# Performance work log

Measured on AMD Instinct MI355X. Metric: run time of the kernel, lower is better.

Reference implementation:

```python
import jax, jax.numpy as jnp
import numpy as np
import math

NUM_HEADS = 16
HEAD_SIZE = 64
SEQ_LEN = 2048
D_MODEL = NUM_HEADS * HEAD_SIZE
BATCH = 2


def _xavier(key, shape):
    fan_in, fan_out = shape[0], shape[1]
    limit = math.sqrt(6.0 / (fan_in + fan_out))
    return jax.random.uniform(key, shape, jnp.float32, -limit, limit)


def setup_inputs() -> dict:
    key = jax.random.key(0)
    ks = jax.random.split(key, 5)
    x = jax.random.normal(ks[0], (BATCH, SEQ_LEN, D_MODEL), jnp.float32)
    W_Q = _xavier(ks[1], (D_MODEL, D_MODEL))
    W_K = _xavier(ks[2], (D_MODEL, D_MODEL))
    W_V = _xavier(ks[3], (D_MODEL, D_MODEL))
    W_O = _xavier(ks[4], (D_MODEL, D_MODEL))
    zeros = jnp.zeros((D_MODEL,), jnp.float32)
    return {
        "x": x,
        "W_Q": W_Q, "W_K": W_K, "W_V": W_V, "W_O": W_O,
        "b_Q": zeros, "b_K": zeros, "b_V": zeros, "b_O": zeros,
    }


def _split_heads(t):
    # [B, S, H*d] -> [B, H, S, d]
    B, S, _ = t.shape
    return t.reshape(B, S, NUM_HEADS, HEAD_SIZE).transpose(0, 2, 1, 3)


def reference(x, W_Q, W_K, W_V, W_O, b_Q, b_K, b_V, b_O):
    q = _split_heads(x @ W_Q + b_Q)  # [B,H,S,d]
    k = _split_heads(x @ W_K + b_K)
    v = _split_heads(x @ W_V + b_V)

    # scores: [B,H,S,S]
    scores = jnp.einsum("bhqd,bhkd->bhqk", q, k)
    # Faithful to original: multiply by lower-triangular 0/1 mask, scale,
    # then add -10000 on strictly-upper positions (NOT -inf).
    tril = jnp.tril(jnp.ones((SEQ_LEN, SEQ_LEN), jnp.float32))
    neg_bias = jnp.triu(jnp.full((SEQ_LEN, SEQ_LEN), -10000.0, jnp.float32), 1)
    masked = scores * tril / np.sqrt(HEAD_SIZE).astype(np.float32) + neg_bias
    weights = jax.nn.softmax(masked, axis=-1)

    hs = jnp.einsum("bhqk,bhkd->bhqd", weights, v)  # [B,H,S,d]
    B = hs.shape[0]
    merged = hs.transpose(0, 2, 1, 3).reshape(B, SEQ_LEN, D_MODEL)
    return merged @ W_O + b_O
```

## Files before the change

### kernel.cpp

```cpp
#include <hip/hip_runtime.h>
#include <hip/hip_bf16.h>

#define S_LEN 2048
#define NH 16
#define HD 64
#define DM 1024
#define BATCH 2
#define M_ROWS (BATCH * S_LEN)
#define SCALE2 0.18033688011112043f
#define M2FIX 8.0f

typedef float f32x4 __attribute__((ext_vector_type(4)));
typedef float f32x16 __attribute__((ext_vector_type(16)));
typedef __bf16 bf16x8 __attribute__((ext_vector_type(8)));
typedef short short8 __attribute__((ext_vector_type(8)));

__device__ __forceinline__ unsigned short f2bf(float f) {
  unsigned u = __builtin_bit_cast(unsigned, f);
  u += 0x7FFFu + ((u >> 16) & 1u);
  return (unsigned short)(u >> 16);
}

__device__ __forceinline__ f32x4 mfma16(bf16x8 a, bf16x8 b, f32x4 c) {
  return __builtin_amdgcn_mfma_f32_16x16x32_bf16(a, b, c, 0, 0, 0);
}

__device__ __forceinline__ f32x16 mfma32(bf16x8 a, bf16x8 b, f32x16 c) {
  return __builtin_amdgcn_mfma_f32_32x32x16_bf16(a, b, c, 0, 0, 0);
}

__device__ __forceinline__ void gload_lds16(const void* g, void* l) {
  __builtin_amdgcn_global_load_lds(
      (const __attribute__((address_space(1))) void*)g,
      (__attribute__((address_space(3))) void*)l, 16, 0, 0);
}

__global__ __launch_bounds__(256) void cast_bf16_kernel(
    const float* __restrict__ in, unsigned short* __restrict__ out) {
  int i = blockIdx.x * 256 + threadIdx.x;
  const float4* p = (const float4*)in;
  float4 f0 = p[i * 2], f1 = p[i * 2 + 1];
  short8 o;
  o[0] = (short)f2bf(f0.x); o[1] = (short)f2bf(f0.y);
  o[2] = (short)f2bf(f0.z); o[3] = (short)f2bf(f0.w);
  o[4] = (short)f2bf(f1.x); o[5] = (short)f2bf(f1.y);
  o[6] = (short)f2bf(f1.z); o[7] = (short)f2bf(f1.w);
  ((short8*)out)[i] = o;
}

__global__ __launch_bounds__(256) void transpose_cast_kernel(
    const float* __restrict__ W0, const float* __restrict__ W1,
    const float* __restrict__ W2, const float* __restrict__ W3,
    unsigned short* __restrict__ out) {
  int z = blockIdx.z;
  const float* W = (z == 0) ? W0 : (z == 1) ? W1 : (z == 2) ? W2 : W3;
  __shared__ float tile[32][33];
  int tx = threadIdx.x & 31, ty = threadIdx.x >> 5;
  int bx = blockIdx.x * 32, by = blockIdx.y * 32;
#pragma unroll
  for (int i = 0; i < 4; ++i)
    tile[ty + i * 8][tx] = W[(size_t)(by + ty + i * 8) * DM + bx + tx];
  __syncthreads();
  unsigned short* o = out + (size_t)z * DM * DM;
#pragma unroll
  for (int i = 0; i < 4; ++i)
    o[(size_t)(bx + ty + i * 8) * DM + by + tx] = f2bf(tile[tx][ty + i * 8]);
}

template <int MODE>
__global__ __launch_bounds__(256) void gemm_bt_kernel(
    const unsigned short* __restrict__ A, const unsigned short* __restrict__ Bt,
    void* __restrict__ Cptr, const float* __restrict__ bias0,
    const float* __restrict__ bias1, const float* __restrict__ bias2,
    int M, int N, int K) {
  __shared__ __align__(16) unsigned short Sbuf[2][3][4096];
  unsigned short (*As)[4096] = Sbuf[0];
  unsigned short (*Bs)[4096] = Sbuf[1];
  const int t = threadIdx.x, lane = t & 63;
  const int wid = t >> 6, wr = wid >> 1, wc = wid & 1;
  const int r16 = lane & 15, g = lane >> 4;
  const int m0 = blockIdx.y * 128, n0 = blockIdx.x * 128;
  const int nk = K >> 5;

  const int n1 = t, n2 = t + 256;
  const int r1g = t >> 2, c1g = (t & 3) * 8;
  const int r2g = (t + 256) >> 2;

  const unsigned short* ap1 = A + (size_t)(m0 + r1g) * K + c1g;
  const unsigned short* ap2 = A + (size_t)(m0 + r2g) * K + c1g;
  const unsigned short* bp1 = Bt + (size_t)(n0 + r1g) * K + c1g;
  const unsigned short* bp2 = Bt + (size_t)(n0 + r2g) * K + c1g;

#define GSTAGE(s)                          \
  gload_lds16(ap1, &As[s][n1 * 8]);        \
  gload_lds16(bp1, &Bs[s][n1 * 8]);        \
  gload_lds16(ap2, &As[s][n2 * 8]);        \
  gload_lds16(bp2, &Bs[s][n2 * 8]);        \
  ap1 += 32; ap2 += 32; bp1 += 32; bp2 += 32;

  f32x4 acc[4][4] = {};

  GSTAGE(0);
  GSTAGE(1);

  for (int kt = 0; kt < nk; ++kt) {
    const int cs = kt % 3;
    if (kt + 1 < nk) {
      asm volatile("s_waitcnt vmcnt(4)" ::: "memory");
    } else {
      asm volatile("s_waitcnt vmcnt(0)" ::: "memory");
    }
    __builtin_amdgcn_s_barrier();
    if (kt + 2 < nk) { GSTAGE((kt + 2) % 3); }

    bf16x8 af[4], bfr[4];
#pragma unroll
    for (int mi = 0; mi < 4; ++mi)
      af[mi] = *(const bf16x8*)&As[cs][(wr * 64 + mi * 16 + r16) * 32 + g * 8];
#pragma unroll
    for (int ni = 0; ni < 4; ++ni)
      bfr[ni] = *(const bf16x8*)&Bs[cs][(wc * 64 + ni * 16 + r16) * 32 + g * 8];
    __builtin_amdgcn_s_setprio(1);
#pragma unroll
    for (int mi = 0; mi < 4; ++mi)
#pragma unroll
      for (int ni = 0; ni < 4; ++ni)
        acc[mi][ni] = mfma16(af[mi], bfr[ni], acc[mi][ni]);
    __builtin_amdgcn_s_setprio(0);
  }
#undef GSTAGE

  if (MODE == 0) {
    unsigned short* Cb = (unsigned short*)Cptr;
    const int buf = n0 >> 10;
    if (buf < 2) {
      const float* bp = buf ? bias1 : bias0;
      const float sc = buf ? 1.0f : SCALE2;
#pragma unroll
      for (int ni = 0; ni < 4; ++ni) {
        int cn = (n0 & 1023) + wc * 64 + ni * 16 + r16;
        float bv = bp[cn];
#pragma unroll
        for (int mi = 0; mi < 4; ++mi) {
          int rowb = m0 + wr * 64 + mi * 16 + 4 * g;
#pragma unroll
          for (int j = 0; j < 4; ++j)
            Cb[(size_t)buf * 4194304u + (size_t)(rowb + j) * 1024 + cn] =
                __builtin_bit_cast(unsigned short, (__bf16)((acc[mi][ni][j] + bv) * sc));
        }
      }
    } else {
      unsigned short* T = &Sbuf[0][0][0];
      __syncthreads();
#pragma unroll
      for (int ni = 0; ni < 4; ++ni) {
        int cnl = wc * 64 + ni * 16 + r16;
        float bv = bias2[(n0 & 1023) + cnl];
#pragma unroll
        for (int mi = 0; mi < 4; ++mi) {
          int sl = wr * 64 + mi * 16 + 4 * g;
          union { __bf16 h4[4]; uint2 u; } cv;
#pragma unroll
          for (int j = 0; j < 4; ++j) cv.h4[j] = (__bf16)(acc[mi][ni][j] + bv);
          *(uint2*)&T[cnl * 136 + sl] = cv.u;
        }
      }
      __syncthreads();
      const int bb = m0 >> 11, s0g = m0 & 2047;
      unsigned short* Vt = Cb + 8388608u;
#pragma unroll
      for (int p = 0; p < 8; ++p) {
        int idx = p * 256 + t;
        int cnl = idx >> 4, sch = idx & 15;
        int cng = (n0 & 1023) + cnl;
        int hh = cng >> 6, d = cng & 63;
        short8 v = *(const short8*)&T[cnl * 136 + sch * 8];
        *(short8*)&Vt[(((size_t)((bb * 16 + hh) * 64 + d)) << 11) + s0g + sch * 8] = v;
      }
    }
  } else {
    float* Cf = (float*)Cptr;
#pragma unroll
    for (int ni = 0; ni < 4; ++ni) {
      int col = n0 + wc * 64 + ni * 16 + r16;
      float bv = bias0[col];
#pragma unroll
      for (int mi = 0; mi < 4; ++mi) {
        int rowb = m0 + wr * 64 + mi * 16 + 4 * g;
#pragma unroll
        for (int j = 0; j < 4; ++j)
          Cf[(size_t)(rowb + j) * N + col] = acc[mi][ni][j] + bv;
      }
    }
  }
}

__global__ __launch_bounds__(256, 2) void attn_kernel(
    const unsigned short* __restrict__ Qm, const unsigned short* __restrict__ Km,
    const unsigned short* __restrict__ VtG, unsigned short* __restrict__ Om) {
  const int t = threadIdx.x, lane = t & 63, w = t >> 6;
  const int l31 = lane & 31, hi = lane >> 5;
  const int bid = blockIdx.x;
  const int xk = bid & 7, slot = bid >> 3;
  const int grp = xk * 4 + (slot >> 4);
  const int mq = slot & 15;
  const int h = grp & 15, b = grp >> 4;

  __shared__ __align__(16) char LB[71680];
  float* R = (float*)LB;
  float* ls = (float*)(LB + 69632);

  const unsigned short* Kbase = Km + (size_t)(b * S_LEN) * DM + h * HD;
  const unsigned short* Vbase = VtG + (size_t)((b * NH + h) * HD) * S_LEN;

  const int kg = ((t & 7) ^ ((t >> 3) & 7)) * 8;
  const int kr0 = t >> 3;
  const int vg = ((t & 15) ^ ((t >> 4) & 15)) * 8;
  const int vr0 = t >> 4;

  auto stage = [&](int cs, int kv0) {
    unsigned short* kd = (unsigned short*)(LB + cs * 16384) + t * 8;
    unsigned short* vd = (unsigned short*)(LB + 32768 + cs * 16384) + t * 8;
#pragma unroll
    for (int p = 0; p < 4; ++p)
      gload_lds16(Kbase + (size_t)(kv0 + kr0 + 32 * p) * DM + kg, kd + 2048 * p);
#pragma unroll
    for (int p = 0; p < 4; ++p)
      gload_lds16(Vbase + (size_t)(vr0 + 16 * p) * S_LEN + kv0 + vg, vd + 2048 * p);
  };

  for (int half = 0; half < 2; ++half) {
    const int T = half ? 31 - mq : mq;
    const int q0 = T * 64;

    bf16x8 qfr[2][4];
#pragma unroll
    for (int qt = 0; qt < 2; ++qt) {
      const unsigned short* Qp =
          Qm + (size_t)(b * S_LEN + q0 + qt * 32 + l31) * DM + h * HD;
#pragma unroll
      for (int kc = 0; kc < 4; ++kc)
        qfr[qt][kc] = *(const bf16x8*)(Qp + kc * 16 + hi * 8);
    }

    f32x16 oacc[2][2] = {};
    float lsum0 = 0.f, lsum1 = 0.f;
    const int ntk = (T >> 1) + 1;

    stage(0, 0);

    for (int kt = 0; kt < ntk; ++kt) {
      const int cs = kt & 1;
      asm volatile("s_waitcnt vmcnt(0)" ::: "memory");
      __builtin_amdgcn_s_barrier();
      if (kt + 1 < ntk) stage(cs ^ 1, (kt + 1) * 128);

      const int kv0w = kt * 128 + w * 32;
      if (kv0w <= q0 + 63) {
        const unsigned short* Ksb = (const unsigned short*)(LB + cs * 16384);
        const unsigned short* Vsb = (const unsigned short*)(LB + 32768 + cs * 16384);

        bf16x8 kf[4];
#pragma unroll
        for (int kc = 0; kc < 4; ++kc)
          kf[kc] = *(const bf16x8*)&Ksb[(w * 32 + l31) * 64 +
                                        (((hi + 2 * kc) ^ (lane & 7)) * 8)];
        bool act0 = false, act1 = false;
        bf16x8 pfr[2][2];
#pragma unroll
        for (int qt = 0; qt < 2; ++qt) {
          const bool act = (kv0w <= q0 + qt * 32 + 31);
          if (qt == 0) act0 = act; else act1 = act;
          if (!act) continue;
          f32x16 st = {};
          __builtin_amdgcn_s_setprio(1);
#pragma unroll
          for (int kc = 0; kc < 4; ++kc) st = mfma32(kf[kc], qfr[qt][kc], st);
          __builtin_amdgcn_s_setprio(0);

          const bool needmask = (kv0w + 31 > q0 + qt * 32);
          const int qg = q0 + qt * 32 + l31;
          float p[16];
          float ps = 0.f;
#pragma unroll
          for (int r = 0; r < 16; ++r) {
            int row = (r & 3) + 8 * (r >> 2) + 4 * hi;
            float v = __builtin_amdgcn_exp2f(st[r] - M2FIX);
            if (needmask && (kv0w + row > qg)) v = 0.f;
            p[r] = v;
            ps += v;
          }
          if (qt == 0) lsum0 += ps; else lsum1 += ps;

          unsigned pw[8];
#pragma unroll
          for (int r = 0; r < 8; ++r) {
            union { __bf16 h2[2]; unsigned u; } cv;
            cv.h2[0] = (__bf16)p[2 * r];
            cv.h2[1] = (__bf16)p[2 * r + 1];
            pw[r] = cv.u;
          }
          {
            auto s0 = __builtin_amdgcn_permlane32_swap(pw[0], pw[2], false, false);
            pw[0] = s0[0]; pw[2] = s0[1];
            auto s1 = __builtin_amdgcn_permlane32_swap(pw[1], pw[3], false, false);
            pw[1] = s1[0]; pw[3] = s1[1];
            auto s2 = __builtin_amdgcn_permlane32_swap(pw[4], pw[6], false, false);
            pw[4] = s2[0]; pw[6] = s2[1];
            auto s3 = __builtin_amdgcn_permlane32_swap(pw[5], pw[7], false, false);
            pw[5] = s3[0]; pw[7] = s3[1];
          }
          union { unsigned u[4]; bf16x8 v; } f0, f1;
          f0.u[0] = pw[0]; f0.u[1] = pw[1]; f0.u[2] = pw[2]; f0.u[3] = pw[3];
          f1.u[0] = pw[4]; f1.u[1] = pw[5]; f1.u[2] = pw[6]; f1.u[3] = pw[7];
          pfr[qt][0] = f0.v;
          pfr[qt][1] = f1.v;
        }

        bf16x8 vf[2][2];
#pragma unroll
        for (int dt = 0; dt < 2; ++dt)
#pragma unroll
          for (int ks = 0; ks < 2; ++ks)
            vf[dt][ks] = *(const bf16x8*)&Vsb[(dt * 32 + l31) * 128 +
                                              (((4 * w + 2 * ks + hi) ^ (lane & 15)) * 8)];
        __builtin_amdgcn_s_setprio(1);
        if (act0) {
#pragma unroll
          for (int dt = 0; dt < 2; ++dt) {
            oacc[dt][0] = mfma32(vf[dt][0], pfr[0][0], oacc[dt][0]);
            oacc[dt][0] = mfma32(vf[dt][1], pfr[0][1], oacc[dt][0]);
          }
        }
        if (act1) {
#pragma unroll
          for (int dt = 0; dt < 2; ++dt) {
            oacc[dt][1] = mfma32(vf[dt][0], pfr[1][0], oacc[dt][1]);
            oacc[dt][1] = mfma32(vf[dt][1], pfr[1][1], oacc[dt][1]);
          }
        }
        __builtin_amdgcn_s_setprio(0);
      }
    }

    __syncthreads();
    float* Rw = R + w * 4352;
#pragma unroll
    for (int dt = 0; dt < 2; ++dt)
#pragma unroll
      for (int qt = 0; qt < 2; ++qt) {
        int q = qt * 32 + l31;
#pragma unroll
        for (int r = 0; r < 16; r += 2) {
          int d = dt * 32 + ((r & 3) + 8 * (r >> 2)) + 4 * hi;
          float2 v2;
          v2.x = oacc[dt][qt][r];
          v2.y = oacc[dt][qt][r + 1];
          *(float2*)&Rw[q * 68 + d] = v2;
        }
      }
    ls[(w * 64 + l31) * 2 + hi] = lsum0;
    ls[(w * 64 + 32 + l31) * 2 + hi] = lsum1;
    __syncthreads();

    const int rq = t >> 2, dq = (t & 3) * 16;
    f32x4 a0 = {}, a1 = {}, a2 = {}, a3 = {};
#pragma unroll
    for (int w4 = 0; w4 < 4; ++w4) {
      const float* Rb = R + w4 * 4352 + rq * 68 + dq;
      a0 += *(const f32x4*)&Rb[0];
      a1 += *(const f32x4*)&Rb[4];
      a2 += *(const f32x4*)&Rb[8];
      a3 += *(const f32x4*)&Rb[12];
    }
    float s = 0.f;
#pragma unroll
    for (int w4 = 0; w4 < 4; ++w4)
      s += ls[(w4 * 64 + rq) * 2] + ls[(w4 * 64 + rq) * 2 + 1];
    float li = 1.0f / s;
    unsigned short* op = Om + (size_t)(b * S_LEN + q0 + rq) * DM + h * HD + dq;
    union { __bf16 hh[8]; uint4 u; } o0, o1;
#pragma unroll
    for (int i = 0; i < 4; ++i) {
      o0.hh[i] = (__bf16)(a0[i] * li);
      o0.hh[4 + i] = (__bf16)(a1[i] * li);
      o1.hh[i] = (__bf16)(a2[i] * li);
      o1.hh[4 + i] = (__bf16)(a3[i] * li);
    }
    *(uint4*)op = o0.u;
    *(uint4*)(op + 8) = o1.u;
    __syncthreads();
  }
}

extern "C" void kernel_launch(void* const* d_in, const int* in_sizes, int n_in,
                              void* d_out, int out_size, void* d_ws, size_t ws_size,
                              hipStream_t stream) {
  (void)in_sizes; (void)n_in; (void)out_size; (void)ws_size;
  const float* x  = (const float*)d_in[0];
  const float* WQ = (const float*)d_in[1];
  const float* WK = (const float*)d_in[2];
  const float* WV = (const float*)d_in[3];
  const float* WO = (const float*)d_in[4];
  const float* bQ = (const float*)d_in[5];
  const float* bK = (const float*)d_in[6];
  const float* bV = (const float*)d_in[7];
  const float* bO = (const float*)d_in[8];

  char* ws = (char*)d_ws;
  unsigned short* xb  = (unsigned short*)(ws);
  unsigned short* wt  = (unsigned short*)(ws + (8u << 20));
  unsigned short* qb  = (unsigned short*)(ws + (16u << 20));
  unsigned short* hsb = (unsigned short*)(ws + (40u << 20));

  cast_bf16_kernel<<<2048, 256, 0, stream>>>(x, xb);
  transpose_cast_kernel<<<dim3(32, 32, 4), 256, 0, stream>>>(WQ, WK, WV, WO, wt);
  gemm_bt_kernel<0><<<dim3(24, 32), 256, 0, stream>>>(
      xb, wt, (void*)qb, bQ, bK, bV, M_ROWS, 3072, DM);
  attn_kernel<<<512, 256, 0, stream>>>(qb, qb + 4194304u, qb + 8388608u, hsb);
  gemm_bt_kernel<1><<<dim3(8, 32), 256, 0, stream>>>(
      hsb, wt + 3u * 1048576u, d_out, bO, nullptr, nullptr, M_ROWS, DM, DM);
}
```

Baseline: 104.0 us.

## Use 256x256 XCD-aware tiles with swizzled LDS for QKV GEMM

Replaces the 128x128 QKV projection GEMM with a 512-thread kernel computing 256x256 tiles over 192 blocks. Blocks are mapped so each XCD handles neighbouring row tiles, and the LDS layout is XOR-swizzled to avoid bank conflicts. The A and B stage loads are split across two MFMA half-phases to overlap them with compute. The output GEMM also gets an XOR-swizzled LDS layout. The larger tiles reduce global traffic per FLOP but may cut occupancy and add barriers, and 192 blocks is fewer than the GPU's CU count.

```diff
diff --git a/kernel.cpp b/kernel.cpp
--- a/kernel.cpp
+++ b/kernel.cpp
@@ -67,15 +67,157 @@
     o[(size_t)(bx + ty + i * 8) * DM + by + tx] = f2bf(tile[tx][ty + i * 8]);
 }
 
-template <int MODE>
-__global__ __launch_bounds__(256) void gemm_bt_kernel(
+__global__ __launch_bounds__(512, 2) void gemm_qkv256_kernel(
     const unsigned short* __restrict__ A, const unsigned short* __restrict__ Bt,
-    void* __restrict__ Cptr, const float* __restrict__ bias0,
-    const float* __restrict__ bias1, const float* __restrict__ bias2,
-    int M, int N, int K) {
-  __shared__ __align__(16) unsigned short Sbuf[2][3][4096];
-  unsigned short (*As)[4096] = Sbuf[0];
-  unsigned short (*Bs)[4096] = Sbuf[1];
+    unsigned short* __restrict__ Cb, const float* __restrict__ bQ,
+    const float* __restrict__ bK, const float* __restrict__ bV) {
+  const int t = threadIdx.x, lane = t & 63;
+  const int wid = t >> 6, wr = wid >> 2, wc = wid & 3;
+  const int r16 = lane & 15, g = lane >> 4;
+  const int K = 1024, nk = 32;
+
+  const int lid = blockIdx.x;
+  const int xcd = lid & 7, idx = lid >> 3;
+  const int by = xcd * 2 + (idx >= 12);
+  const int bx = (idx >= 12) ? idx - 12 : idx;
+  const int m0 = by * 256, n0 = bx * 256;
+
+  __shared__ __align__(16) char LB[98304];
+
+  const int c0 = t, c1 = t + 512;
+  const int pr0 = c0 >> 3, v0 = (c0 & 7) ^ (pr0 & 7);
+  const int pr1 = c1 >> 3, v1 = (c1 & 7) ^ (pr1 & 7);
+  const int ar0 = 2 * pr0 + (v0 >> 2), ak0 = (v0 & 3) * 8;
+  const int ar1 = 2 * pr1 + (v1 >> 2), ak1 = (v1 & 3) * 8;
+
+#define ASLOT(s) ((unsigned short*)(LB + (s) * 16384))
+#define BSLOT(s) ((unsigned short*)(LB + 49152 + (s) * 16384))
+#define STAGE_A(s, k0)                                                        \
+  gload_lds16(A + (size_t)(m0 + ar0) * K + (k0) + ak0, ASLOT(s) + c0 * 8);    \
+  gload_lds16(A + (size_t)(m0 + ar1) * K + (k0) + ak1, ASLOT(s) + c1 * 8);
+#define STAGE_B(s, k0)                                                        \
+  gload_lds16(Bt + (size_t)(n0 + ar0) * K + (k0) + ak0, BSLOT(s) + c0 * 8);   \
+  gload_lds16(Bt + (size_t)(n0 + ar1) * K + (k0) + ak1, BSLOT(s) + c1 * 8);
+
+  const int S16 = ((r16 & 1) * 4 + g) ^ (r16 >> 1);
+  const int aoff = (r16 >> 1) * 128 + S16 * 16;
+
+  f32x4 acc[8][4] = {};
+
+  STAGE_A(0, 0); STAGE_B(0, 0);
+  STAGE_A(1, 32); STAGE_B(1, 32);
+  asm volatile("s_waitcnt vmcnt(4)" ::: "memory");
+  __builtin_amdgcn_s_barrier();
+
+  for (int j = 0; j < nk; ++j) {
+    const int cs = j % 3, ps = (j + 2) % 3;
+    const char* As_ = (const char*)ASLOT(cs);
+    const char* Bs_ = (const char*)BSLOT(cs);
+
+    bf16x8 af[4], bf[4];
+#pragma unroll
+    for (int mi = 0; mi < 4; ++mi)
+      af[mi] = *(const bf16x8*)(As_ + (wr * 64 + mi * 8) * 128 + aoff);
+#pragma unroll
+    for (int ni = 0; ni < 4; ++ni)
+      bf[ni] = *(const bf16x8*)(Bs_ + (wc * 32 + ni * 8) * 128 + aoff);
+    if (j + 2 < nk) { STAGE_A(ps, (j + 2) * 32); }
+    __builtin_amdgcn_s_barrier();
+    asm volatile("s_waitcnt lgkmcnt(0)" ::: "memory");
+    __builtin_amdgcn_s_setprio(1);
+#pragma unroll
+    for (int mi = 0; mi < 4; ++mi)
+#pragma unroll
+      for (int ni = 0; ni < 4; ++ni)
+        acc[mi][ni] = mfma16(af[mi], bf[ni], acc[mi][ni]);
+    __builtin_amdgcn_s_setprio(0);
+    __builtin_amdgcn_s_barrier();
+
+    bf16x8 af2[4];
+#pragma unroll
+    for (int mi = 0; mi < 4; ++mi)
+      af2[mi] = *(const bf16x8*)(As_ + (wr * 64 + 32 + mi * 8) * 128 + aoff);
+    if (j + 2 < nk) { STAGE_B(ps, (j + 2) * 32); }
+    __builtin_amdgcn_s_barrier();
+    asm volatile("s_waitcnt lgkmcnt(0)" ::: "memory");
+    __builtin_amdgcn_s_setprio(1);
+#pragma unroll
+    for (int mi = 0; mi < 4; ++mi)
+#pragma unroll
+      for (int ni = 0; ni < 4; ++ni)
+        acc[4 + mi][ni] = mfma16(af2[mi], bf[ni], acc[4 + mi][ni]);
+    __builtin_amdgcn_s_setprio(0);
+
+    if (j + 1 < nk) {
+      if (j + 2 < nk) {
+        asm volatile("s_waitcnt vmcnt(4)" ::: "memory");
+      } else {
+        asm volatile("s_waitcnt vmcnt(0)" ::: "memory");
+      }
+    }
+    __builtin_amdgcn_s_barrier();
+  }
+#undef STAGE_A
+#undef STAGE_B
+
+  const int bufq = n0 >> 10;
+  if (bufq < 2) {
+    const float* bp = bufq ? bK : bQ;
+    const float sc = bufq ? 1.0f : SCALE2;
+#pragma unroll
+    for (int ni = 0; ni < 4; ++ni) {
+      int cn = (n0 & 1023) + wc * 64 + ni * 16 + r16;
+      float bv = bp[cn];
+#pragma unroll
+      for (int mi = 0; mi < 8; ++mi) {
+        int row = m0 + wr * 128 + mi * 16 + 4 * g;
+#pragma unroll
+        for (int jj = 0; jj < 4; ++jj)
+          Cb[(size_t)bufq * 4194304u + (size_t)(row + jj) * 1024 + cn] =
+              __builtin_bit_cast(unsigned short, (__bf16)((acc[mi][ni][jj] + bv) * sc));
+      }
+    }
+  } else {
+    unsigned short* T = (unsigned short*)LB;
+    const int bb = m0 >> 11, s0g = m0 & 2047;
+    unsigned short* Vt = Cb + 8388608u;
+#pragma unroll
+    for (int ph = 0; ph < 2; ++ph) {
+      __syncthreads();
+      if ((wc >> 1) == ph) {
+#pragma unroll
+        for (int ni = 0; ni < 4; ++ni) {
+          int cnl = (wc & 1) * 64 + ni * 16 + r16;
+          float bv = bV[(n0 & 1023) + ph * 128 + cnl];
+#pragma unroll
+          for (int mi = 0; mi < 8; ++mi) {
+            int sl = wr * 128 + mi * 16 + 4 * g;
+            union { __bf16 h4[4]; uint2 u; } cv;
+#pragma unroll
+            for (int jj = 0; jj < 4; ++jj) cv.h4[jj] = (__bf16)(acc[mi][ni][jj] + bv);
+            *(uint2*)&T[cnl * 264 + sl] = cv.u;
+          }
+        }
+      }
+      __syncthreads();
+#pragma unroll
+      for (int q = 0; q < 8; ++q) {
+        int idx2 = q * 512 + t;
+        int cnl = idx2 >> 5, sch = idx2 & 31;
+        int cng = (n0 & 1023) + ph * 128 + cnl;
+        int hh = cng >> 6, d = cng & 63;
+        short8 v = *(const short8*)&T[cnl * 264 + sch * 8];
+        *(short8*)&Vt[(((size_t)((bb * 16 + hh) * 64 + d)) << 11) + s0g + sch * 8] = v;
+      }
+    }
+  }
+}
+
+__global__ __launch_bounds__(256) void gemm_out_kernel(
+    const unsigned short* __restrict__ A, const unsigned short* __restrict__ Bt,
+    float* __restrict__ Cf, const float* __restrict__ bias0, int M, int N, int K) {
+  __shared__ __align__(16) unsigned short As[3][4096];
+  __shared__ __align__(16) unsigned short Bs[3][4096];
   const int t = threadIdx.x, lane = t & 63;
   const int wid = t >> 6, wr = wid >> 1, wc = wid & 1;
   const int r16 = lane & 15, g = lane >> 4;
@@ -83,8 +225,9 @@
   const int nk = K >> 5;
 
   const int n1 = t, n2 = t + 256;
-  const int r1g = t >> 2, c1g = (t & 3) * 8;
-  const int r2g = (t + 256) >> 2;
+  const int r1g = t >> 2;
+  const int r2g = r1g + 64;
+  const int c1g = ((t & 3) ^ (r1g & 3)) * 8;
 
   const unsigned short* ap1 = A + (size_t)(m0 + r1g) * K + c1g;
   const unsigned short* ap2 = A + (size_t)(m0 + r2g) * K + c1g;
@@ -99,9 +242,10 @@
   ap1 += 32; ap2 += 32; bp1 += 32; bp2 += 32;
 
   f32x4 acc[4][4] = {};
-
   GSTAGE(0);
   GSTAGE(1);
+
+  const int axr = ((g ^ (r16 & 3)) * 8);
 
   for (int kt = 0; kt < nk; ++kt) {
     const int cs = kt % 3;
@@ -116,10 +260,10 @@
     bf16x8 af[4], bfr[4];
 #pragma unroll
     for (int mi = 0; mi < 4; ++mi)
-      af[mi] = *(const bf16x8*)&As[cs][(wr * 64 + mi * 16 + r16) * 32 + g * 8];
+      af[mi] = *(const bf16x8*)&As[cs][(wr * 64 + mi * 16 + r16) * 32 + axr];
 #pragma unroll
     for (int ni = 0; ni < 4; ++ni)
-      bfr[ni] = *(const bf16x8*)&Bs[cs][(wc * 64 + ni * 16 + r16) * 32 + g * 8];
+      bfr[ni] = *(const bf16x8*)&Bs[cs][(wc * 64 + ni * 16 + r16) * 32 + axr];
     __builtin_amdgcn_s_setprio(1);
 #pragma unroll
     for (int mi = 0; mi < 4; ++mi)
@@ -130,67 +274,16 @@
   }
 #undef GSTAGE
 
-  if (MODE == 0) {
-    unsigned short* Cb = (unsigned short*)Cptr;
-    const int buf = n0 >> 10;
-    if (buf < 2) {
-      const float* bp = buf ? bias1 : bias0;
-      const float sc = buf ? 1.0f : SCALE2;
-#pragma unroll
-      for (int ni = 0; ni < 4; ++ni) {
-        int cn = (n0 & 1023) + wc * 64 + ni * 16 + r16;
-        float bv = bp[cn];
-#pragma unroll
-        for (int mi = 0; mi < 4; ++mi) {
-          int rowb = m0 + wr * 64 + mi * 16 + 4 * g;
-#pragma unroll
-          for (int j = 0; j < 4; ++j)
-            Cb[(size_t)buf * 4194304u + (size_t)(rowb + j) * 1024 + cn] =
-                __builtin_bit_cast(unsigned short, (__bf16)((acc[mi][ni][j] + bv) * sc));
-        }
-      }
-    } else {
-      unsigned short* T = &Sbuf[0][0][0];
-      __syncthreads();
-#pragma unroll
-      for (int ni = 0; ni < 4; ++ni) {
-        int cnl = wc * 64 + ni * 16 + r16;
-        float bv = bias2[(n0 & 1023) + cnl];
-#pragma unroll
-        for (int mi = 0; mi < 4; ++mi) {
-          int sl = wr * 64 + mi * 16 + 4 * g;
-          union { __bf16 h4[4]; uint2 u; } cv;
-#pragma unroll
-          for (int j = 0; j < 4; ++j) cv.h4[j] = (__bf16)(acc[mi][ni][j] + bv);
-          *(uint2*)&T[cnl * 136 + sl] = cv.u;
-        }
-      }
-      __syncthreads();
-      const int bb = m0 >> 11, s0g = m0 & 2047;
-      unsigned short* Vt = Cb + 8388608u;
-#pragma unroll
-      for (int p = 0; p < 8; ++p) {
-        int idx = p * 256 + t;
-        int cnl = idx >> 4, sch = idx & 15;
-        int cng = (n0 & 1023) + cnl;
-        int hh = cng >> 6, d = cng & 63;
-        short8 v = *(const short8*)&T[cnl * 136 + sch * 8];
-        *(short8*)&Vt[(((size_t)((bb * 16 + hh) * 64 + d)) << 11) + s0g + sch * 8] = v;
-      }
-    }
-  } else {
-    float* Cf = (float*)Cptr;
-#pragma unroll
-    for (int ni = 0; ni < 4; ++ni) {
-      int col = n0 + wc * 64 + ni * 16 + r16;
-      float bv = bias0[col];
-#pragma unroll
-      for (int mi = 0; mi < 4; ++mi) {
-        int rowb = m0 + wr * 64 + mi * 16 + 4 * g;
-#pragma unroll
-        for (int j = 0; j < 4; ++j)
-          Cf[(size_t)(rowb + j) * N + col] = acc[mi][ni][j] + bv;
-      }
+#pragma unroll
+  for (int ni = 0; ni < 4; ++ni) {
+    int col = n0 + wc * 64 + ni * 16 + r16;
+    float bv = bias0[col];
+#pragma unroll
+    for (int mi = 0; mi < 4; ++mi) {
+      int rowb = m0 + wr * 64 + mi * 16 + 4 * g;
+#pragma unroll
+      for (int j = 0; j < 4; ++j)
+        Cf[(size_t)(rowb + j) * N + col] = acc[mi][ni][j] + bv;
     }
   }
 }
@@ -415,9 +508,8 @@
 
   cast_bf16_kernel<<<2048, 256, 0, stream>>>(x, xb);
   transpose_cast_kernel<<<dim3(32, 32, 4), 256, 0, stream>>>(WQ, WK, WV, WO, wt);
-  gemm_bt_kernel<0><<<dim3(24, 32), 256, 0, stream>>>(
-      xb, wt, (void*)qb, bQ, bK, bV, M_ROWS, 3072, DM);
+  gemm_qkv256_kernel<<<192, 512, 0, stream>>>(xb, wt, qb, bQ, bK, bV);
   attn_kernel<<<512, 256, 0, stream>>>(qb, qb + 4194304u, qb + 8388608u, hsb);
-  gemm_bt_kernel<1><<<dim3(8, 32), 256, 0, stream>>>(
-      hsb, wt + 3u * 1048576u, d_out, bO, nullptr, nullptr, M_ROWS, DM, DM);
-}
+  gemm_out_kernel<<<dim3(8, 32), 256, 0, stream>>>(
+      hsb, wt + 3u * 1048576u, (float*)d_out, bO, M_ROWS, DM, DM);
+}
```

Measured after the change: 110.3 us. +6.1%, slower.
